# Kernel tuning notes

Hardware: AMD Instinct MI355X
Metric: run time of the kernel (lower is better)

Reference implementation:

```python
import jax, jax.numpy as jnp
import numpy as np
import math

D, H, NQP, NKP = 512, 8, 4, 4
DH = D // H
OUT_DIM = D + H * NKP * 3  # 608


def setup_inputs() -> dict:
    key = jax.random.key(0)
    ks = jax.random.split(key, 12)
    B, L = 2, 1024
    s = jax.random.normal(ks[0], (B, L, D), dtype=jnp.float32)
    R = jax.random.normal(ks[1], (B, L, 3, 3), dtype=jnp.float32)
    tr = jax.random.normal(ks[2], (B, L, 3), dtype=jnp.float32)
    sc = 0.02
    Wq = jax.random.normal(ks[3], (D, D), dtype=jnp.float32) * sc
    Wk = jax.random.normal(ks[4], (D, D), dtype=jnp.float32) * sc
    Wv = jax.random.normal(ks[5], (D, D), dtype=jnp.float32) * sc
    Wqp = jax.random.normal(ks[6], (D, H * NQP * 3), dtype=jnp.float32) * sc
    Wkp = jax.random.normal(ks[7], (D, H * NKP * 3), dtype=jnp.float32) * sc
    Wvp = jax.random.normal(ks[8], (D, H * NKP * 3), dtype=jnp.float32) * sc
    Wo = jax.random.normal(ks[9], (OUT_DIM, D), dtype=jnp.float32) * sc
    bo = jnp.zeros((D,), dtype=jnp.float32)
    gamma = jnp.ones((D,), dtype=jnp.float32)
    beta = jnp.zeros((D,), dtype=jnp.float32)
    w_C = jnp.full((H,), math.log(20.0), dtype=jnp.float32)
    return dict(s=s, R=R, tr=tr, Wq=Wq, Wk=Wk, Wv=Wv, Wqp=Wqp, Wkp=Wkp,
                Wvp=Wvp, Wo=Wo, bo=bo, gamma=gamma, beta=beta, w_C=w_C)


def _layernorm(x, gamma, beta, eps=1e-5):
    mu = jnp.mean(x, axis=-1, keepdims=True)
    var = jnp.var(x, axis=-1, keepdims=True)
    return (x - mu) * jax.lax.rsqrt(var + eps) * gamma + beta


def reference(s, R, tr, Wq, Wk, Wv, Wqp, Wkp, Wvp, Wo, bo, gamma, beta, w_C):
    B, L, _ = s.shape
    # scalar q/k/v: (B, L, H, dh)
    Q = (s @ Wq).reshape(B, L, H, DH)
    K = (s @ Wk).reshape(B, L, H, DH)
    V = (s @ Wv).reshape(B, L, H, DH)
    a_s = jnp.einsum('bihd,bjhd->bhij', Q, K) / math.sqrt(DH)
    # local points: (B, L, H, P, 3)
    Qp = (s @ Wqp).reshape(B, L, H, NQP, 3)
    Kp = (s @ Wkp).reshape(B, L, H, NKP, 3)
    Vp = (s @ Wvp).reshape(B, L, H, NKP, 3)
    tr_e = tr[:, :, None, None, :]
    to_global = lambda p: jnp.einsum('blxy,blhpy->blhpx', R, p) + tr_e
    Qp_g, Kp_g, Vp_g = to_global(Qp), to_global(Kp), to_global(Vp)
    # (B, H, L, P, 3)
    qh = jnp.transpose(Qp_g, (0, 2, 1, 3, 4))
    kh = jnp.transpose(Kp_g, (0, 2, 1, 3, 4))
    diff = qh[:, :, :, None] - kh[:, :, None]          # (B,H,L,L,P,3)
    sq_dist = jnp.sum(diff * diff, axis=(-2, -1))      # (B,H,L,L)
    wc = jax.nn.softplus(w_C)[None, :, None, None]
    attn = jax.nn.softmax(a_s - 0.5 * wc * sq_dist, axis=-1)
    out_s = jnp.einsum('bhij,bjhd->bihd', attn, V).reshape(B, L, D)
    Vp_agg = jnp.einsum('bhij,bjhpc->bihpc', attn, Vp_g)  # (B,L,H,P,3)
    # global -> local: R^T (p - tr)
    Vp_local = jnp.einsum('blyx,blhpy->blhpx', R, Vp_agg - tr_e)
    out_p = Vp_local.reshape(B, L, H * NKP * 3)
    out = jnp.concatenate([out_s, out_p], axis=-1) @ Wo + bo
    return _layernorm(s + out, gamma, beta)
```

## Files before the change

### kernel.cpp

```cpp
#include <hip/hip_runtime.h>
#include <hip/hip_fp16.h>
#include <math.h>

typedef _Float16 f16;
typedef _Float16 f16x8 __attribute__((ext_vector_type(8)));
typedef _Float16 f16x4v __attribute__((ext_vector_type(4)));
typedef float f32x4 __attribute__((ext_vector_type(4)));

#define BATCH   2
#define LSEQ    1024
#define BLTOT   2048
#define DMODEL  512
#define NHEAD   8
#define PDIM    1824
#define AW      96
#define VW      80
#define ODIM    608
#define NSPLIT  2
#define OCPSTR  1310720

__global__ __launch_bounds__(256)
void prep_kernel(const float* __restrict__ Wq, const float* __restrict__ Wk,
                 const float* __restrict__ Wv, const float* __restrict__ Wqp,
                 const float* __restrict__ Wkp, const float* __restrict__ Wvp,
                 const float* __restrict__ Wo,
                 f16* __restrict__ WallT, f16* __restrict__ WoT)
{
    const int blk = blockIdx.x;
    const int t = threadIdx.x;
    __shared__ float tile[32][33];

    if (blk < 912) {
        const int n0 = (blk % 57) * 32, k0 = (blk / 57) * 32;
        const float* src; int ld, nc0;
        if      (n0 < 512)  { src = Wq;  ld = 512; nc0 = n0; }
        else if (n0 < 1024) { src = Wk;  ld = 512; nc0 = n0 - 512; }
        else if (n0 < 1536) { src = Wv;  ld = 512; nc0 = n0 - 1024; }
        else if (n0 < 1632) { src = Wqp; ld = 96;  nc0 = n0 - 1536; }
        else if (n0 < 1728) { src = Wkp; ld = 96;  nc0 = n0 - 1632; }
        else                { src = Wvp; ld = 96;  nc0 = n0 - 1728; }
#pragma unroll
        for (int i = 0; i < 4; ++i) {
            const int idx2 = t + i * 256;
            const int kl = idx2 >> 5, nl = idx2 & 31;
            tile[kl][nl] = src[(long long)(k0 + kl) * ld + nc0 + nl];
        }
        __syncthreads();
#pragma unroll
        for (int i = 0; i < 4; ++i) {
            const int idx2 = t + i * 256;
            const int nl = idx2 >> 5, kl = idx2 & 31;
            WallT[(long long)(n0 + nl) * 512 + k0 + kl] = (f16)tile[kl][nl];
        }
        return;
    }
    {
        const int idx = blk - 912;
        const int n0 = (idx % 16) * 32, k0 = (idx / 16) * 32;
#pragma unroll
        for (int i = 0; i < 4; ++i) {
            const int idx2 = t + i * 256;
            const int kl = idx2 >> 5, nl = idx2 & 31;
            tile[kl][nl] = Wo[(long long)(k0 + kl) * 512 + n0 + nl];
        }
        __syncthreads();
#pragma unroll
        for (int i = 0; i < 4; ++i) {
            const int idx2 = t + i * 256;
            const int nl = idx2 >> 5, kl = idx2 & 31;
            WoT[(long long)(n0 + nl) * 608 + k0 + kl] = (f16)tile[kl][nl];
        }
    }
}

__global__ __launch_bounds__(256)
void proj_kernel(const float* __restrict__ s, const f16* __restrict__ WallT,
                 f16* __restrict__ P)
{
    __shared__ f16 As[2][128][40];
    __shared__ f16 Bs[2][96][40];
    const int t = threadIdx.x;
    const int w = t >> 6, lane = t & 63, l15 = lane & 15, lhi = lane >> 4;
    const int row0 = blockIdx.y * 128, col0 = blockIdx.x * 96;

    f32x4 acc[2][6];
#pragma unroll
    for (int m = 0; m < 2; ++m)
#pragma unroll
        for (int n = 0; n < 6; ++n) acc[m][n] = (f32x4){0.f, 0.f, 0.f, 0.f};

    float4 aR[2][2];
    f16x8 bR[2];

#pragma unroll
    for (int i = 0; i < 2; ++i) {
        const int cid = t + i * 256;
        const int r = cid >> 2, c = cid & 3;
        aR[i][0] = *(const float4*)&s[(long long)(row0 + r) * 512 + c * 8];
        aR[i][1] = *(const float4*)&s[(long long)(row0 + r) * 512 + c * 8 + 4];
    }
#pragma unroll
    for (int i = 0; i < 2; ++i) {
        const int cid = t + i * 256;
        if (cid < 384) {
            const int br = cid >> 2, bc = cid & 3;
            bR[i] = *(const f16x8*)&WallT[(long long)(col0 + br) * 512 + bc * 8];
        }
    }
#pragma unroll
    for (int i = 0; i < 2; ++i) {
        const int cid = t + i * 256;
        const int r = cid >> 2, c = cid & 3;
        f16x8 v = { (f16)aR[i][0].x, (f16)aR[i][0].y, (f16)aR[i][0].z, (f16)aR[i][0].w,
                    (f16)aR[i][1].x, (f16)aR[i][1].y, (f16)aR[i][1].z, (f16)aR[i][1].w };
        *(f16x8*)&As[0][r][c * 8] = v;
    }
#pragma unroll
    for (int i = 0; i < 2; ++i) {
        const int cid = t + i * 256;
        if (cid < 384) *(f16x8*)&Bs[0][cid >> 2][(cid & 3) * 8] = bR[i];
    }
    __syncthreads();

    for (int st = 0; st < 16; ++st) {
        const int cur = st & 1;
        if (st + 1 < 16) {
            const int k0 = (st + 1) << 5;
#pragma unroll
            for (int i = 0; i < 2; ++i) {
                const int cid = t + i * 256;
                const int r = cid >> 2, c = cid & 3;
                aR[i][0] = *(const float4*)&s[(long long)(row0 + r) * 512 + k0 + c * 8];
                aR[i][1] = *(const float4*)&s[(long long)(row0 + r) * 512 + k0 + c * 8 + 4];
            }
#pragma unroll
            for (int i = 0; i < 2; ++i) {
                const int cid = t + i * 256;
                if (cid < 384) {
                    const int br = cid >> 2, bc = cid & 3;
                    bR[i] = *(const f16x8*)&WallT[(long long)(col0 + br) * 512 + k0 + bc * 8];
                }
            }
        }
        f16x8 af[2], bf[6];
#pragma unroll
        for (int m = 0; m < 2; ++m)
            af[m] = *(const f16x8*)&As[cur][w * 32 + m * 16 + l15][lhi * 8];
#pragma unroll
        for (int n = 0; n < 6; ++n)
            bf[n] = *(const f16x8*)&Bs[cur][n * 16 + l15][lhi * 8];
#pragma unroll
        for (int m = 0; m < 2; ++m)
#pragma unroll
            for (int n = 0; n < 6; ++n)
                acc[m][n] = __builtin_amdgcn_mfma_f32_16x16x32_f16(af[m], bf[n], acc[m][n], 0, 0, 0);
        if (st + 1 < 16) {
#pragma unroll
            for (int i = 0; i < 2; ++i) {
                const int cid = t + i * 256;
                const int r = cid >> 2, c = cid & 3;
                f16x8 v = { (f16)aR[i][0].x, (f16)aR[i][0].y, (f16)aR[i][0].z, (f16)aR[i][0].w,
                            (f16)aR[i][1].x, (f16)aR[i][1].y, (f16)aR[i][1].z, (f16)aR[i][1].w };
                *(f16x8*)&As[cur ^ 1][r][c * 8] = v;
            }
#pragma unroll
            for (int i = 0; i < 2; ++i) {
                const int cid = t + i * 256;
                if (cid < 384) *(f16x8*)&Bs[cur ^ 1][cid >> 2][(cid & 3) * 8] = bR[i];
            }
        }
        __syncthreads();
    }

#pragma unroll
    for (int m = 0; m < 2; ++m) {
        const int row = row0 + w * 32 + m * 16 + lhi * 4;
#pragma unroll
        for (int n = 0; n < 6; ++n) {
            const int col = col0 + n * 16 + l15;
#pragma unroll
            for (int r = 0; r < 4; ++r)
                P[(long long)(row + r) * PDIM + col] = (f16)acc[m][n][r];
        }
    }
}

__global__ __launch_bounds__(256)
void build_aug2_kernel(const f16* __restrict__ P, const float* __restrict__ Rm,
                       const float* __restrict__ tr, const float* __restrict__ wC,
                       f16* __restrict__ QA, f16* __restrict__ KA,
                       f16* __restrict__ VCT, float* __restrict__ KOFF)
{
    const int l0 = blockIdx.x * 64;
    const int bh = blockIdx.y;
    const int b = bh >> 3, h = bh & 7;
    const int t = threadIdx.x;

    __shared__ float Rl[64][9];
    __shared__ float trl[64][3];
    __shared__ f16 gq[64][12];
    __shared__ f16 gk[64][12];
    __shared__ float k2[64][4];
    __shared__ f16 Vt[VW][72];
    __shared__ float wcs;

    const long long blbase = (long long)b * LSEQ + l0;

    for (int i = t; i < 64 * 9; i += 256) Rl[i / 9][i % 9] = Rm[blbase * 9 + i];
    for (int i = t; i < 64 * 3; i += 256) trl[i / 3][i % 3] = tr[blbase * 3 + i];
    if (t == 0) { float x = wC[h]; wcs = log1pf(expf(x)); }
    __syncthreads();
    const float wc = wcs;

    for (int i = t; i < 768; i += 256) {
        const int l = i / 12, pp = i - l * 12;
        const int proj = pp >> 2, p = pp & 3;
        const f16* src = P + (blbase + l) * PDIM + 1536 + proj * 96 + h * 12 + p * 3;
        const float x = (float)src[0], y = (float)src[1], z = (float)src[2];
        const float gx = Rl[l][0]*x + Rl[l][1]*y + Rl[l][2]*z + trl[l][0];
        const float gy = Rl[l][3]*x + Rl[l][4]*y + Rl[l][5]*z + trl[l][1];
        const float gz = Rl[l][6]*x + Rl[l][7]*y + Rl[l][8]*z + trl[l][2];
        if (proj == 0) {
            gq[l][p * 3 + 0] = (f16)(wc * gx);
            gq[l][p * 3 + 1] = (f16)(wc * gy);
            gq[l][p * 3 + 2] = (f16)(wc * gz);
        } else if (proj == 1) {
            gk[l][p * 3 + 0] = (f16)gx;
            gk[l][p * 3 + 1] = (f16)gy;
            gk[l][p * 3 + 2] = (f16)gz;
            k2[l][p] = gx * gx + gy * gy + gz * gz;
        } else {
            Vt[64 + p * 3 + 0][l] = (f16)gx;
            Vt[64 + p * 3 + 1][l] = (f16)gy;
            Vt[64 + p * 3 + 2][l] = (f16)gz;
        }
    }
    for (int i = t; i < 512; i += 256) {
        const int l = i >> 3, ch = i & 7;
        f16x8 v = *(const f16x8*)&P[(blbase + l) * PDIM + 1024 + h * 64 + ch * 8];
#pragma unroll
        for (int j = 0; j < 8; ++j) Vt[ch * 8 + j][l] = v[j];
    }
    for (int i = t; i < 36; i += 256) {
        const int r = 76 + i / 9, ch = i % 9;
        *(f16x8*)&Vt[r][ch * 8] = (f16x8){0,0,0,0,0,0,0,0};
    }
    __syncthreads();

    if (t < 64)
        KOFF[(long long)bh * LSEQ + l0 + t] =
            0.5f * wc * (k2[t][0] + k2[t][1] + k2[t][2] + k2[t][3]);

    for (int i = t; i < 768; i += 256) {
        const int l = i / 12, ch = i - l * 12;
        const long long prow = (blbase + l) * PDIM;
        const long long orow = ((long long)bh * LSEQ + l0 + l) * AW;
        f16x8 q, k;
        if (ch < 8) {
            f16x8 qv = *(const f16x8*)&P[prow + h * 64 + ch * 8];
            f16x8 kv = *(const f16x8*)&P[prow + 512 + h * 64 + ch * 8];
            q = qv * (f16)0.125f;
            k = kv;
        } else if (ch == 8) {
#pragma unroll
            for (int j = 0; j < 8; ++j) { q[j] = gq[l][j]; k[j] = gk[l][j]; }
        } else if (ch == 9) {
#pragma unroll
            for (int j = 0; j < 8; ++j) {
                q[j] = (j < 4) ? gq[l][8 + j] : (f16)0.f;
                k[j] = (j < 4) ? gk[l][8 + j] : (f16)0.f;
            }
        } else {
            q = (f16x8){0,0,0,0,0,0,0,0};
            k = (f16x8){0,0,0,0,0,0,0,0};
        }
        *(f16x8*)&QA[orow + ch * 8] = q;
        *(f16x8*)&KA[orow + ch * 8] = k;
    }
    for (int i = t; i < 640; i += 256) {
        const int c = i >> 3, lg = i & 7;
        *(f16x8*)&VCT[((long long)bh * VW + c) * LSEQ + l0 + lg * 8] =
            *(const f16x8*)&Vt[c][lg * 8];
    }
}

__global__ __launch_bounds__(256, 2)
void attn_kernel(const f16* __restrict__ QA, const f16* __restrict__ KA,
                 const f16* __restrict__ VCT, const float* __restrict__ KOFF,
                 f16* __restrict__ OCp, float* __restrict__ LSE)
{
    const int bh = blockIdx.y;
    const int q0 = blockIdx.x * 64;
    const int z  = blockIdx.z;
    const int t = threadIdx.x;
    const int w = t >> 6, lane = t & 63, l15 = lane & 15, lhi = lane >> 4;

    __shared__ f16 Ks[128][104];
    __shared__ f16 Vs[VW][136];
    __shared__ f16 Ps[64][136];

    const f16* qbase = QA + ((long long)bh * LSEQ + q0 + w * 16 + l15) * AW;
    f16x8 qf[3];
#pragma unroll
    for (int ks = 0; ks < 3; ++ks)
        qf[ks] = *(const f16x8*)(qbase + ks * 32 + lhi * 8);

    f32x4 Oacc[5];
#pragma unroll
    for (int nv = 0; nv < 5; ++nv) Oacc[nv] = (f32x4){0.f, 0.f, 0.f, 0.f};
    float M[4], L[4];
#pragma unroll
    for (int r = 0; r < 4; ++r) { M[r] = -1e30f; L[r] = 0.f; }

    const f16* kgbase = KA + (long long)bh * LSEQ * AW;
    const f16* vgbase = VCT + (long long)bh * VW * LSEQ;
    const float* koffb = KOFF + (long long)bh * LSEQ;

    const int kvbeg = z * (LSEQ / NSPLIT);
    const int kvend = kvbeg + LSEQ / NSPLIT;

#pragma unroll
    for (int i = 0; i < 6; ++i) {
        const int cid = t + i * 256;
        const int r = cid / 12, c = cid - r * 12;
        *(f16x8*)&Ks[r][c * 8] = *(const f16x8*)(kgbase + (long long)(kvbeg + r) * AW + c * 8);
    }
#pragma unroll
    for (int i = 0; i < 5; ++i) {
        const int cid = t + i * 256;
        const int r = cid >> 4, c = cid & 15;
        *(f16x8*)&Vs[r][c * 8] = *(const f16x8*)(vgbase + (long long)r * LSEQ + kvbeg + c * 8);
    }
    __syncthreads();

    for (int kv0 = kvbeg; kv0 < kvend; kv0 += 128) {
        const bool more = (kv0 + 128 < kvend);
        f16x8 kpre[6], vpre[5];
        if (more) {
#pragma unroll
            for (int i = 0; i < 6; ++i) {
                const int cid = t + i * 256;
                const int r = cid / 12, c = cid - r * 12;
                kpre[i] = *(const f16x8*)(kgbase + (long long)(kv0 + 128 + r) * AW + c * 8);
            }
#pragma unroll
            for (int i = 0; i < 5; ++i) {
                const int cid = t + i * 256;
                const int r = cid >> 4, c = cid & 15;
                vpre[i] = *(const f16x8*)(vgbase + (long long)r * LSEQ + kv0 + 128 + c * 8);
            }
        }

        f32x4 sc[8];
#pragma unroll
        for (int n = 0; n < 8; ++n) sc[n] = (f32x4){0.f, 0.f, 0.f, 0.f};
        __builtin_amdgcn_s_setprio(1);
#pragma unroll
        for (int n = 0; n < 8; ++n)
#pragma unroll
            for (int ks = 0; ks < 3; ++ks) {
                f16x8 kb = *(const f16x8*)&Ks[n * 16 + l15][ks * 32 + lhi * 8];
                sc[n] = __builtin_amdgcn_mfma_f32_16x16x32_f16(qf[ks], kb, sc[n], 0, 0, 0);
            }
        __builtin_amdgcn_s_setprio(0);
#pragma unroll
        for (int n = 0; n < 8; ++n) {
            const float ko = koffb[kv0 + n * 16 + l15];
#pragma unroll
            for (int r = 0; r < 4; ++r) sc[n][r] -= ko;
        }
        float mr[4];
#pragma unroll
        for (int r = 0; r < 4; ++r) {
            float m = sc[0][r];
#pragma unroll
            for (int n = 1; n < 8; ++n) m = fmaxf(m, sc[n][r]);
#pragma unroll
            for (int off = 1; off < 16; off <<= 1) m = fmaxf(m, __shfl_xor(m, off));
            mr[r] = m;
        }
        const bool nog = (mr[0] <= M[0] + 8.f) && (mr[1] <= M[1] + 8.f) &&
                         (mr[2] <= M[2] + 8.f) && (mr[3] <= M[3] + 8.f);
        float rsum[4] = {0.f, 0.f, 0.f, 0.f};
        if (__all(nog)) {
#pragma unroll
            for (int n = 0; n < 8; ++n)
#pragma unroll
                for (int r = 0; r < 4; ++r) {
                    const float p = __expf(sc[n][r] - M[r]);
                    sc[n][r] = p;
                    rsum[r] += p;
                }
#pragma unroll
            for (int r = 0; r < 4; ++r) {
                float s2 = rsum[r];
#pragma unroll
                for (int off = 1; off < 16; off <<= 1) s2 += __shfl_xor(s2, off);
                L[r] += s2;
            }
        } else {
            float sscale[4];
#pragma unroll
            for (int r = 0; r < 4; ++r) {
                const float nm = fmaxf(M[r], mr[r]);
                sscale[r] = __expf(M[r] - nm);
                M[r] = nm;
            }
#pragma unroll
            for (int n = 0; n < 8; ++n)
#pragma unroll
                for (int r = 0; r < 4; ++r) {
                    const float p = __expf(sc[n][r] - M[r]);
                    sc[n][r] = p;
                    rsum[r] += p;
                }
#pragma unroll
            for (int r = 0; r < 4; ++r) {
                float s2 = rsum[r];
#pragma unroll
                for (int off = 1; off < 16; off <<= 1) s2 += __shfl_xor(s2, off);
                L[r] = L[r] * sscale[r] + s2;
            }
#pragma unroll
            for (int nv = 0; nv < 5; ++nv)
#pragma unroll
                for (int r = 0; r < 4; ++r) Oacc[nv][r] *= sscale[r];
        }

#pragma unroll
        for (int n = 0; n < 8; ++n)
#pragma unroll
            for (int r = 0; r < 4; ++r)
                Ps[w * 16 + lhi * 4 + r][n * 16 + l15] = (f16)sc[n][r];

        f16x8 pa[4];
#pragma unroll
        for (int ks = 0; ks < 4; ++ks)
            pa[ks] = *(const f16x8*)&Ps[w * 16 + l15][ks * 32 + lhi * 8];
        __builtin_amdgcn_s_setprio(1);
#pragma unroll
        for (int nv = 0; nv < 5; ++nv)
#pragma unroll
            for (int ks = 0; ks < 4; ++ks) {
                f16x8 vb = *(const f16x8*)&Vs[nv * 16 + l15][ks * 32 + lhi * 8];
                Oacc[nv] = __builtin_amdgcn_mfma_f32_16x16x32_f16(pa[ks], vb, Oacc[nv], 0, 0, 0);
            }
        __builtin_amdgcn_s_setprio(0);
        __syncthreads();

        if (more) {
#pragma unroll
            for (int i = 0; i < 6; ++i) {
                const int cid = t + i * 256;
                const int r = cid / 12, c = cid - r * 12;
                *(f16x8*)&Ks[r][c * 8] = kpre[i];
            }
#pragma unroll
            for (int i = 0; i < 5; ++i) {
                const int cid = t + i * 256;
                const int r = cid >> 4, c = cid & 15;
                *(f16x8*)&Vs[r][c * 8] = vpre[i];
            }
        }
        __syncthreads();
    }

    float inv[4];
#pragma unroll
    for (int r = 0; r < 4; ++r) inv[r] = 1.0f / L[r];
    f16* obase = OCp + (((long long)(z * 16 + bh) * LSEQ) + q0 + w * 16 + lhi * 4) * VW;
#pragma unroll
    for (int nv = 0; nv < 5; ++nv)
#pragma unroll
        for (int r = 0; r < 4; ++r)
            obase[r * VW + nv * 16 + l15] = (f16)(Oacc[nv][r] * inv[r]);
    if (l15 == 0) {
#pragma unroll
        for (int r = 0; r < 4; ++r)
            LSE[(long long)(z * 16 + bh) * LSEQ + q0 + w * 16 + lhi * 4 + r] =
                M[r] + __logf(L[r]);
    }
}

__global__ __launch_bounds__(256)
void combine_concat_kernel(const f16* __restrict__ OCp, const float* __restrict__ LSE,
                           const float* __restrict__ Rm, const float* __restrict__ tr,
                           f16* __restrict__ CC)
{
    const int bl0 = blockIdx.x * 4;
    const int b = bl0 >> 10;
    const int t = threadIdx.x;

    __shared__ float w1s[4][8], w2s[4][8];
    if (t < 32) {
        const int row = t >> 3, h = t & 7;
        const int l = (bl0 + row) & 1023;
        const int bh = b * 8 + h;
        const float l1 = LSE[(long long)bh * LSEQ + l];
        const float l2 = LSE[(long long)(16 + bh) * LSEQ + l];
        const float mm = fmaxf(l1, l2);
        const float e1 = __expf(l1 - mm), e2 = __expf(l2 - mm);
        const float inv = 1.0f / (e1 + e2);
        w1s[row][h] = e1 * inv; w2s[row][h] = e2 * inv;
    }
    __syncthreads();

    for (int idx = t; idx < 2048; idx += 256) {
        const int row = idx >> 9, c = idx & 511;
        const int h = c >> 6, ch = c & 63;
        const int l = (bl0 + row) & 1023;
        const long long base = ((long long)(b * 8 + h) * LSEQ + l) * VW + ch;
        const float v = w1s[row][h] * (float)OCp[base] + w2s[row][h] * (float)OCp[OCPSTR + base];
        CC[(long long)(bl0 + row) * ODIM + c] = (f16)v;
    }
    if (t < 128) {
        const int row = t >> 5, h = (t >> 2) & 7, p = t & 3;
        const int bl = bl0 + row, l = bl & 1023;
        const long long base = ((long long)(b * 8 + h) * LSEQ + l) * VW + 64 + p * 3;
        const float w1 = w1s[row][h], w2 = w2s[row][h];
        float o[3];
#pragma unroll
        for (int c = 0; c < 3; ++c)
            o[c] = w1 * (float)OCp[base + c] + w2 * (float)OCp[OCPSTR + base + c]
                 - tr[(long long)bl * 3 + c];
        const float* Rr = Rm + (long long)bl * 9;
        f16* crow = CC + (long long)bl * ODIM + 512 + h * 12 + p * 3;
        crow[0] = (f16)(Rr[0]*o[0] + Rr[3]*o[1] + Rr[6]*o[2]);
        crow[1] = (f16)(Rr[1]*o[0] + Rr[4]*o[1] + Rr[7]*o[2]);
        crow[2] = (f16)(Rr[2]*o[0] + Rr[5]*o[1] + Rr[8]*o[2]);
    }
}

__global__ __launch_bounds__(256)
void out_gemm_kernel(const f16* __restrict__ CC, const f16* __restrict__ WoT,
                     float* __restrict__ Y)
{
    __shared__ f16 As[2][64][40];
    __shared__ f16 Bs[2][64][40];
    const int t = threadIdx.x;
    const int w = t >> 6, lane = t & 63, l15 = lane & 15, lhi = lane >> 4;
    const int wr = w >> 1, wc = w & 1;
    const int row0 = blockIdx.y * 64, col0 = blockIdx.x * 64;
    const int ar = t >> 2, ac = t & 3;

    f32x4 acc[2][2];
#pragma unroll
    for (int m = 0; m < 2; ++m)
#pragma unroll
        for (int n = 0; n < 2; ++n) acc[m][n] = (f32x4){0.f, 0.f, 0.f, 0.f};

    f16x8 aR, bR;
    aR = *(const f16x8*)&CC[(long long)(row0 + ar) * ODIM + ac * 8];
    bR = *(const f16x8*)&WoT[(long long)(col0 + ar) * ODIM + ac * 8];
    *(f16x8*)&As[0][ar][ac * 8] = aR;
    *(f16x8*)&Bs[0][ar][ac * 8] = bR;
    __syncthreads();

    for (int st = 0; st < 19; ++st) {
        const int cur = st & 1;
        if (st + 1 < 19) {
            const int k0 = (st + 1) << 5;
            aR = *(const f16x8*)&CC[(long long)(row0 + ar) * ODIM + k0 + ac * 8];
            bR = *(const f16x8*)&WoT[(long long)(col0 + ar) * ODIM + k0 + ac * 8];
        }
        f16x8 af[2], bf[2];
#pragma unroll
        for (int m = 0; m < 2; ++m)
            af[m] = *(const f16x8*)&As[cur][wr * 32 + m * 16 + l15][lhi * 8];
#pragma unroll
        for (int n = 0; n < 2; ++n)
            bf[n] = *(const f16x8*)&Bs[cur][wc * 32 + n * 16 + l15][lhi * 8];
#pragma unroll
        for (int m = 0; m < 2; ++m)
#pragma unroll
            for (int n = 0; n < 2; ++n)
                acc[m][n] = __builtin_amdgcn_mfma_f32_16x16x32_f16(af[m], bf[n], acc[m][n], 0, 0, 0);
        if (st + 1 < 19) {
            *(f16x8*)&As[cur ^ 1][ar][ac * 8] = aR;
            *(f16x8*)&Bs[cur ^ 1][ar][ac * 8] = bR;
        }
        __syncthreads();
    }

#pragma unroll
    for (int m = 0; m < 2; ++m) {
        const int row = row0 + wr * 32 + m * 16 + lhi * 4;
#pragma unroll
        for (int n = 0; n < 2; ++n) {
            const int col = col0 + wc * 32 + n * 16 + l15;
#pragma unroll
            for (int r = 0; r < 4; ++r)
                Y[(long long)(row + r) * 512 + col] = acc[m][n][r];
        }
    }
}

__global__ __launch_bounds__(256)
void residual_ln_kernel(const float* __restrict__ s, const float* __restrict__ Y,
                        const float* __restrict__ bo, const float* __restrict__ gamma,
                        const float* __restrict__ beta, float* __restrict__ out)
{
    const int bl = blockIdx.x;
    const int t = threadIdx.x;
    const float* srow = s + (long long)bl * DMODEL;
    const float* yrow = Y + (long long)bl * DMODEL;

    const float v0 = srow[t]       + yrow[t]       + bo[t];
    const float v1 = srow[t + 256] + yrow[t + 256] + bo[t + 256];

    float sum = v0 + v1, sq = v0 * v0 + v1 * v1;
#pragma unroll
    for (int o = 32; o > 0; o >>= 1) {
        sum += __shfl_xor(sum, o);
        sq  += __shfl_xor(sq,  o);
    }
    __shared__ float rs[4], rq[4];
    const int wid = t >> 6, lane = t & 63;
    if (lane == 0) { rs[wid] = sum; rq[wid] = sq; }
    __syncthreads();
    sum = rs[0] + rs[1] + rs[2] + rs[3];
    sq  = rq[0] + rq[1] + rq[2] + rq[3];

    const float mu  = sum * (1.0f / DMODEL);
    const float var = sq * (1.0f / DMODEL) - mu * mu;
    const float inv = rsqrtf(var + 1e-5f);

    out[(long long)bl * DMODEL + t]       = (v0 - mu) * inv * gamma[t]       + beta[t];
    out[(long long)bl * DMODEL + t + 256] = (v1 - mu) * inv * gamma[t + 256] + beta[t + 256];
}

extern "C" void kernel_launch(void* const* d_in, const int* in_sizes, int n_in,
                              void* d_out, int out_size, void* d_ws, size_t ws_size,
                              hipStream_t stream)
{
    const float* s    = (const float*)d_in[0];
    const float* R    = (const float*)d_in[1];
    const float* tr   = (const float*)d_in[2];
    const float* Wq   = (const float*)d_in[3];
    const float* Wk   = (const float*)d_in[4];
    const float* Wv   = (const float*)d_in[5];
    const float* Wqp  = (const float*)d_in[6];
    const float* Wkp  = (const float*)d_in[7];
    const float* Wvp  = (const float*)d_in[8];
    const float* Wo   = (const float*)d_in[9];
    const float* bo   = (const float*)d_in[10];
    const float* gam  = (const float*)d_in[11];
    const float* bet  = (const float*)d_in[12];
    const float* wC   = (const float*)d_in[13];
    float* out = (float*)d_out;

    f16* WallT = (f16*)d_ws;
    f16* WoT   = WallT + 933888;
    f16* P     = WoT + 311296;
    f16* QA    = P + 3735552;
    f16* KA    = QA + 1572864;
    f16* VCT   = KA + 1572864;
    float* KOFF = (float*)(VCT + 1310720);
    f16* OCp    = (f16*)(KOFF + 16384);
    float* LSE  = (float*)(OCp + 2621440);
    f16* CC     = (f16*)(LSE + 32768);
    float* Y    = (float*)(CC + 1245184);

    const dim3 blk(256);

    prep_kernel<<<dim3(1216), blk, 0, stream>>>(Wq, Wk, Wv, Wqp, Wkp, Wvp, Wo,
                                                WallT, WoT);

    proj_kernel<<<dim3(19, 16), blk, 0, stream>>>(s, WallT, P);

    build_aug2_kernel<<<dim3(16, 16), blk, 0, stream>>>(P, R, tr, wC, QA, KA, VCT, KOFF);

    attn_kernel<<<dim3(16, 16, NSPLIT), blk, 0, stream>>>(QA, KA, VCT, KOFF, OCp, LSE);

    combine_concat_kernel<<<dim3(512), blk, 0, stream>>>(OCp, LSE, R, tr, CC);

    out_gemm_kernel<<<dim3(8, 32), blk, 0, stream>>>(CC, WoT, Y);

    residual_ln_kernel<<<dim3(BLTOT), blk, 0, stream>>>(s, Y, bo, gam, bet, out);
}
```

Measured before the change: 74.19 us.

## Fuse weight prep into GEMMs and merge split-KV attention with combine

Removes the separate weight transpose/convert kernel: the projection and output GEMMs now load fp32 weights directly and transpose-convert into shared memory per tile. The attention kernel runs both KV halves in one 512-thread block, two groups of four waves. The halves are merged in shared memory and the concat output, including the rotation back to local frames, is written directly. This drops the combine kernel and the partial-output round trip. Costs are scattered 2-byte shared stores for the weight transpose and a larger shared-memory footprint per attention block, which may lower occupancy.

```diff
diff --git a/kernel.cpp b/kernel.cpp
--- a/kernel.cpp
+++ b/kernel.cpp
@@ -16,65 +16,12 @@
 #define AW      96
 #define VW      80
 #define ODIM    608
-#define NSPLIT  2
-#define OCPSTR  1310720
 
 __global__ __launch_bounds__(256)
-void prep_kernel(const float* __restrict__ Wq, const float* __restrict__ Wk,
+void proj_kernel(const float* __restrict__ s,
+                 const float* __restrict__ Wq, const float* __restrict__ Wk,
                  const float* __restrict__ Wv, const float* __restrict__ Wqp,
                  const float* __restrict__ Wkp, const float* __restrict__ Wvp,
-                 const float* __restrict__ Wo,
-                 f16* __restrict__ WallT, f16* __restrict__ WoT)
-{
-    const int blk = blockIdx.x;
-    const int t = threadIdx.x;
-    __shared__ float tile[32][33];
-
-    if (blk < 912) {
-        const int n0 = (blk % 57) * 32, k0 = (blk / 57) * 32;
-        const float* src; int ld, nc0;
-        if      (n0 < 512)  { src = Wq;  ld = 512; nc0 = n0; }
-        else if (n0 < 1024) { src = Wk;  ld = 512; nc0 = n0 - 512; }
-        else if (n0 < 1536) { src = Wv;  ld = 512; nc0 = n0 - 1024; }
-        else if (n0 < 1632) { src = Wqp; ld = 96;  nc0 = n0 - 1536; }
-        else if (n0 < 1728) { src = Wkp; ld = 96;  nc0 = n0 - 1632; }
-        else                { src = Wvp; ld = 96;  nc0 = n0 - 1728; }
-#pragma unroll
-        for (int i = 0; i < 4; ++i) {
-            const int idx2 = t + i * 256;
-            const int kl = idx2 >> 5, nl = idx2 & 31;
-            tile[kl][nl] = src[(long long)(k0 + kl) * ld + nc0 + nl];
-        }
-        __syncthreads();
-#pragma unroll
-        for (int i = 0; i < 4; ++i) {
-            const int idx2 = t + i * 256;
-            const int nl = idx2 >> 5, kl = idx2 & 31;
-            WallT[(long long)(n0 + nl) * 512 + k0 + kl] = (f16)tile[kl][nl];
-        }
-        return;
-    }
-    {
-        const int idx = blk - 912;
-        const int n0 = (idx % 16) * 32, k0 = (idx / 16) * 32;
-#pragma unroll
-        for (int i = 0; i < 4; ++i) {
-            const int idx2 = t + i * 256;
-            const int kl = idx2 >> 5, nl = idx2 & 31;
-            tile[kl][nl] = Wo[(long long)(k0 + kl) * 512 + n0 + nl];
-        }
-        __syncthreads();
-#pragma unroll
-        for (int i = 0; i < 4; ++i) {
-            const int idx2 = t + i * 256;
-            const int nl = idx2 >> 5, kl = idx2 & 31;
-            WoT[(long long)(n0 + nl) * 608 + k0 + kl] = (f16)tile[kl][nl];
-        }
-    }
-}
-
-__global__ __launch_bounds__(256)
-void proj_kernel(const float* __restrict__ s, const f16* __restrict__ WallT,
                  f16* __restrict__ P)
 {
     __shared__ f16 As[2][128][40];
@@ -83,14 +30,29 @@
     const int w = t >> 6, lane = t & 63, l15 = lane & 15, lhi = lane >> 4;
     const int row0 = blockIdx.y * 128, col0 = blockIdx.x * 96;
 
+    const float* bsrc[3]; int bld[3], bkk[3], bnn[3];
+#pragma unroll
+    for (int i = 0; i < 3; ++i) {
+        const int cid = t + i * 256;
+        const int kk = cid / 24, c4 = cid % 24;
+        const int n = col0 + c4 * 4;
+        const float* src; int nc, ld;
+        if      (n < 512)  { src = Wq;  nc = n;        ld = 512; }
+        else if (n < 1024) { src = Wk;  nc = n - 512;  ld = 512; }
+        else if (n < 1536) { src = Wv;  nc = n - 1024; ld = 512; }
+        else if (n < 1632) { src = Wqp; nc = n - 1536; ld = 96; }
+        else if (n < 1728) { src = Wkp; nc = n - 1632; ld = 96; }
+        else               { src = Wvp; nc = n - 1728; ld = 96; }
+        bsrc[i] = src + nc; bld[i] = ld; bkk[i] = kk; bnn[i] = c4 * 4;
+    }
+
     f32x4 acc[2][6];
 #pragma unroll
     for (int m = 0; m < 2; ++m)
 #pragma unroll
         for (int n = 0; n < 6; ++n) acc[m][n] = (f32x4){0.f, 0.f, 0.f, 0.f};
 
-    float4 aR[2][2];
-    f16x8 bR[2];
+    float4 aR[2][2], bpre[3];
 
 #pragma unroll
     for (int i = 0; i < 2; ++i) {
@@ -100,13 +62,8 @@
         aR[i][1] = *(const float4*)&s[(long long)(row0 + r) * 512 + c * 8 + 4];
     }
 #pragma unroll
-    for (int i = 0; i < 2; ++i) {
-        const int cid = t + i * 256;
-        if (cid < 384) {
-            const int br = cid >> 2, bc = cid & 3;
-            bR[i] = *(const f16x8*)&WallT[(long long)(col0 + br) * 512 + bc * 8];
-        }
-    }
+    for (int i = 0; i < 3; ++i)
+        bpre[i] = *(const float4*)&bsrc[i][(long long)bkk[i] * bld[i]];
 #pragma unroll
     for (int i = 0; i < 2; ++i) {
         const int cid = t + i * 256;
@@ -116,9 +73,11 @@
         *(f16x8*)&As[0][r][c * 8] = v;
     }
 #pragma unroll
-    for (int i = 0; i < 2; ++i) {
-        const int cid = t + i * 256;
-        if (cid < 384) *(f16x8*)&Bs[0][cid >> 2][(cid & 3) * 8] = bR[i];
+    for (int i = 0; i < 3; ++i) {
+        Bs[0][bnn[i] + 0][bkk[i]] = (f16)bpre[i].x;
+        Bs[0][bnn[i] + 1][bkk[i]] = (f16)bpre[i].y;
+        Bs[0][bnn[i] + 2][bkk[i]] = (f16)bpre[i].z;
+        Bs[0][bnn[i] + 3][bkk[i]] = (f16)bpre[i].w;
     }
     __syncthreads();
 
@@ -134,13 +93,8 @@
                 aR[i][1] = *(const float4*)&s[(long long)(row0 + r) * 512 + k0 + c * 8 + 4];
             }
 #pragma unroll
-            for (int i = 0; i < 2; ++i) {
-                const int cid = t + i * 256;
-                if (cid < 384) {
-                    const int br = cid >> 2, bc = cid & 3;
-                    bR[i] = *(const f16x8*)&WallT[(long long)(col0 + br) * 512 + k0 + bc * 8];
-                }
-            }
+            for (int i = 0; i < 3; ++i)
+                bpre[i] = *(const float4*)&bsrc[i][(long long)(k0 + bkk[i]) * bld[i]];
         }
         f16x8 af[2], bf[6];
 #pragma unroll
@@ -164,9 +118,11 @@
                 *(f16x8*)&As[cur ^ 1][r][c * 8] = v;
             }
 #pragma unroll
-            for (int i = 0; i < 2; ++i) {
-                const int cid = t + i * 256;
-                if (cid < 384) *(f16x8*)&Bs[cur ^ 1][cid >> 2][(cid & 3) * 8] = bR[i];
+            for (int i = 0; i < 3; ++i) {
+                Bs[cur ^ 1][bnn[i] + 0][bkk[i]] = (f16)bpre[i].x;
+                Bs[cur ^ 1][bnn[i] + 1][bkk[i]] = (f16)bpre[i].y;
+                Bs[cur ^ 1][bnn[i] + 2][bkk[i]] = (f16)bpre[i].z;
+                Bs[cur ^ 1][bnn[i] + 3][bkk[i]] = (f16)bpre[i].w;
             }
         }
         __syncthreads();
@@ -284,22 +240,34 @@
     }
 }
 
-__global__ __launch_bounds__(256, 2)
-void attn_kernel(const f16* __restrict__ QA, const f16* __restrict__ KA,
-                 const f16* __restrict__ VCT, const float* __restrict__ KOFF,
-                 f16* __restrict__ OCp, float* __restrict__ LSE)
+__global__ __launch_bounds__(512, 2)
+void attn8_kernel(const f16* __restrict__ QA, const f16* __restrict__ KA,
+                  const f16* __restrict__ VCT, const float* __restrict__ KOFF,
+                  const float* __restrict__ Rm, const float* __restrict__ trv,
+                  f16* __restrict__ CC)
 {
     const int bh = blockIdx.y;
     const int q0 = blockIdx.x * 64;
-    const int z  = blockIdx.z;
+    const int b = bh >> 3, h = bh & 7;
     const int t = threadIdx.x;
-    const int w = t >> 6, lane = t & 63, l15 = lane & 15, lhi = lane >> 4;
-
-    __shared__ f16 Ks[128][104];
-    __shared__ f16 Vs[VW][136];
-    __shared__ f16 Ps[64][136];
-
-    const f16* qbase = QA + ((long long)bh * LSEQ + q0 + w * 16 + l15) * AW;
+    const int w = t >> 6;
+    const int g = w >> 2;
+    const int wsub = w & 3;
+    const int lane = t & 63, l15 = lane & 15, lhi = lane >> 4;
+    const int tg = t & 255;
+
+    __shared__ f16 Ks[2][128][104];
+    __shared__ f16 Vs[2][VW][136];
+    __shared__ f16 Ps[2][64][136];
+    __shared__ float Rtr[64][12];
+
+    const long long blbase = (long long)b * LSEQ + q0;
+    for (int i = t; i < 64 * 12; i += 512) {
+        const int row = i / 12, c = i % 12;
+        Rtr[row][c] = (c < 9) ? Rm[(blbase + row) * 9 + c] : trv[(blbase + row) * 3 + (c - 9)];
+    }
+
+    const f16* qbase = QA + ((long long)bh * LSEQ + q0 + wsub * 16 + l15) * AW;
     f16x8 qf[3];
 #pragma unroll
     for (int ks = 0; ks < 3; ++ks)
@@ -316,36 +284,36 @@
     const f16* vgbase = VCT + (long long)bh * VW * LSEQ;
     const float* koffb = KOFF + (long long)bh * LSEQ;
 
-    const int kvbeg = z * (LSEQ / NSPLIT);
-    const int kvend = kvbeg + LSEQ / NSPLIT;
+    const int kvbeg = g * 512;
 
 #pragma unroll
     for (int i = 0; i < 6; ++i) {
-        const int cid = t + i * 256;
+        const int cid = tg + i * 256;
         const int r = cid / 12, c = cid - r * 12;
-        *(f16x8*)&Ks[r][c * 8] = *(const f16x8*)(kgbase + (long long)(kvbeg + r) * AW + c * 8);
+        *(f16x8*)&Ks[g][r][c * 8] = *(const f16x8*)(kgbase + (long long)(kvbeg + r) * AW + c * 8);
     }
 #pragma unroll
     for (int i = 0; i < 5; ++i) {
-        const int cid = t + i * 256;
+        const int cid = tg + i * 256;
         const int r = cid >> 4, c = cid & 15;
-        *(f16x8*)&Vs[r][c * 8] = *(const f16x8*)(vgbase + (long long)r * LSEQ + kvbeg + c * 8);
-    }
-    __syncthreads();
-
-    for (int kv0 = kvbeg; kv0 < kvend; kv0 += 128) {
-        const bool more = (kv0 + 128 < kvend);
+        *(f16x8*)&Vs[g][r][c * 8] = *(const f16x8*)(vgbase + (long long)r * LSEQ + kvbeg + c * 8);
+    }
+    __syncthreads();
+
+    for (int it = 0; it < 4; ++it) {
+        const int kv0 = kvbeg + it * 128;
+        const bool more = (it < 3);
         f16x8 kpre[6], vpre[5];
         if (more) {
 #pragma unroll
             for (int i = 0; i < 6; ++i) {
-                const int cid = t + i * 256;
+                const int cid = tg + i * 256;
                 const int r = cid / 12, c = cid - r * 12;
                 kpre[i] = *(const f16x8*)(kgbase + (long long)(kv0 + 128 + r) * AW + c * 8);
             }
 #pragma unroll
             for (int i = 0; i < 5; ++i) {
-                const int cid = t + i * 256;
+                const int cid = tg + i * 256;
                 const int r = cid >> 4, c = cid & 15;
                 vpre[i] = *(const f16x8*)(vgbase + (long long)r * LSEQ + kv0 + 128 + c * 8);
             }
@@ -359,7 +327,7 @@
         for (int n = 0; n < 8; ++n)
 #pragma unroll
             for (int ks = 0; ks < 3; ++ks) {
-                f16x8 kb = *(const f16x8*)&Ks[n * 16 + l15][ks * 32 + lhi * 8];
+                f16x8 kb = *(const f16x8*)&Ks[g][n * 16 + l15][ks * 32 + lhi * 8];
                 sc[n] = __builtin_amdgcn_mfma_f32_16x16x32_f16(qf[ks], kb, sc[n], 0, 0, 0);
             }
         __builtin_amdgcn_s_setprio(0);
@@ -431,18 +399,18 @@
         for (int n = 0; n < 8; ++n)
 #pragma unroll
             for (int r = 0; r < 4; ++r)
-                Ps[w * 16 + lhi * 4 + r][n * 16 + l15] = (f16)sc[n][r];
+                Ps[g][wsub * 16 + lhi * 4 + r][n * 16 + l15] = (f16)sc[n][r];
 
         f16x8 pa[4];
 #pragma unroll
         for (int ks = 0; ks < 4; ++ks)
-            pa[ks] = *(const f16x8*)&Ps[w * 16 + l15][ks * 32 + lhi * 8];
+            pa[ks] = *(const f16x8*)&Ps[g][wsub * 16 + l15][ks * 32 + lhi * 8];
         __builtin_amdgcn_s_setprio(1);
 #pragma unroll
         for (int nv = 0; nv < 5; ++nv)
 #pragma unroll
             for (int ks = 0; ks < 4; ++ks) {
-                f16x8 vb = *(const f16x8*)&Vs[nv * 16 + l15][ks * 32 + lhi * 8];
+                f16x8 vb = *(const f16x8*)&Vs[g][nv * 16 + l15][ks * 32 + lhi * 8];
                 Oacc[nv] = __builtin_amdgcn_mfma_f32_16x16x32_f16(pa[ks], vb, Oacc[nv], 0, 0, 0);
             }
         __builtin_amdgcn_s_setprio(0);
@@ -451,88 +419,69 @@
         if (more) {
 #pragma unroll
             for (int i = 0; i < 6; ++i) {
-                const int cid = t + i * 256;
+                const int cid = tg + i * 256;
                 const int r = cid / 12, c = cid - r * 12;
-                *(f16x8*)&Ks[r][c * 8] = kpre[i];
+                *(f16x8*)&Ks[g][r][c * 8] = kpre[i];
             }
 #pragma unroll
             for (int i = 0; i < 5; ++i) {
-                const int cid = t + i * 256;
+                const int cid = tg + i * 256;
                 const int r = cid >> 4, c = cid & 15;
-                *(f16x8*)&Vs[r][c * 8] = vpre[i];
+                *(f16x8*)&Vs[g][r][c * 8] = vpre[i];
             }
         }
         __syncthreads();
     }
 
-    float inv[4];
-#pragma unroll
-    for (int r = 0; r < 4; ++r) inv[r] = 1.0f / L[r];
-    f16* obase = OCp + (((long long)(z * 16 + bh) * LSEQ) + q0 + w * 16 + lhi * 4) * VW;
-#pragma unroll
-    for (int nv = 0; nv < 5; ++nv)
-#pragma unroll
-        for (int r = 0; r < 4; ++r)
-            obase[r * VW + nv * 16 + l15] = (f16)(Oacc[nv][r] * inv[r]);
-    if (l15 == 0) {
-#pragma unroll
-        for (int r = 0; r < 4; ++r)
-            LSE[(long long)(z * 16 + bh) * LSEQ + q0 + w * 16 + lhi * 4 + r] =
-                M[r] + __logf(L[r]);
+    float* O1  = (float*)&Ks[0][0][0];
+    float* ML1 = O1 + 64 * VW;
+    if (g == 1) {
+#pragma unroll
+        for (int r = 0; r < 4; ++r) {
+            const int i = wsub * 16 + lhi * 4 + r;
+#pragma unroll
+            for (int nv = 0; nv < 5; ++nv)
+                O1[i * VW + nv * 16 + l15] = Oacc[nv][r];
+            if (l15 == 0) { ML1[i * 2 + 0] = M[r]; ML1[i * 2 + 1] = L[r]; }
+        }
+    }
+    __syncthreads();
+
+    float* opbuf = (float*)&Vs[0][0][0];
+    if (g == 0) {
+#pragma unroll
+        for (int r = 0; r < 4; ++r) {
+            const int i = wsub * 16 + lhi * 4 + r;
+            const float m1 = ML1[i * 2 + 0], l1 = ML1[i * 2 + 1];
+            const float nm = fmaxf(M[r], m1);
+            const float a0 = __expf(M[r] - nm), a1 = __expf(m1 - nm);
+            const float inv = 1.0f / (L[r] * a0 + l1 * a1);
+            f16* crow = CC + (blbase + i) * ODIM;
+#pragma unroll
+            for (int nv = 0; nv < 4; ++nv) {
+                const float val = (Oacc[nv][r] * a0 + O1[i * VW + nv * 16 + l15] * a1) * inv;
+                crow[h * 64 + nv * 16 + l15] = (f16)val;
+            }
+            const float val4 = (Oacc[4][r] * a0 + O1[i * VW + 64 + l15] * a1) * inv;
+            if (l15 < 12) opbuf[i * 12 + l15] = val4;
+        }
+    }
+    __syncthreads();
+
+    if (t < 256) {
+        const int i = t >> 2, p = t & 3;
+        const float ox = opbuf[i * 12 + p * 3 + 0] - Rtr[i][9];
+        const float oy = opbuf[i * 12 + p * 3 + 1] - Rtr[i][10];
+        const float oz = opbuf[i * 12 + p * 3 + 2] - Rtr[i][11];
+        f16* crow = CC + (blbase + i) * ODIM + 512 + h * 12 + p * 3;
+        crow[0] = (f16)(Rtr[i][0]*ox + Rtr[i][3]*oy + Rtr[i][6]*oz);
+        crow[1] = (f16)(Rtr[i][1]*ox + Rtr[i][4]*oy + Rtr[i][7]*oz);
+        crow[2] = (f16)(Rtr[i][2]*ox + Rtr[i][5]*oy + Rtr[i][8]*oz);
     }
 }
 
 __global__ __launch_bounds__(256)
-void combine_concat_kernel(const f16* __restrict__ OCp, const float* __restrict__ LSE,
-                           const float* __restrict__ Rm, const float* __restrict__ tr,
-                           f16* __restrict__ CC)
-{
-    const int bl0 = blockIdx.x * 4;
-    const int b = bl0 >> 10;
-    const int t = threadIdx.x;
-
-    __shared__ float w1s[4][8], w2s[4][8];
-    if (t < 32) {
-        const int row = t >> 3, h = t & 7;
-        const int l = (bl0 + row) & 1023;
-        const int bh = b * 8 + h;
-        const float l1 = LSE[(long long)bh * LSEQ + l];
-        const float l2 = LSE[(long long)(16 + bh) * LSEQ + l];
-        const float mm = fmaxf(l1, l2);
-        const float e1 = __expf(l1 - mm), e2 = __expf(l2 - mm);
-        const float inv = 1.0f / (e1 + e2);
-        w1s[row][h] = e1 * inv; w2s[row][h] = e2 * inv;
-    }
-    __syncthreads();
-
-    for (int idx = t; idx < 2048; idx += 256) {
-        const int row = idx >> 9, c = idx & 511;
-        const int h = c >> 6, ch = c & 63;
-        const int l = (bl0 + row) & 1023;
-        const long long base = ((long long)(b * 8 + h) * LSEQ + l) * VW + ch;
-        const float v = w1s[row][h] * (float)OCp[base] + w2s[row][h] * (float)OCp[OCPSTR + base];
-        CC[(long long)(bl0 + row) * ODIM + c] = (f16)v;
-    }
-    if (t < 128) {
-        const int row = t >> 5, h = (t >> 2) & 7, p = t & 3;
-        const int bl = bl0 + row, l = bl & 1023;
-        const long long base = ((long long)(b * 8 + h) * LSEQ + l) * VW + 64 + p * 3;
-        const float w1 = w1s[row][h], w2 = w2s[row][h];
-        float o[3];
-#pragma unroll
-        for (int c = 0; c < 3; ++c)
-            o[c] = w1 * (float)OCp[base + c] + w2 * (float)OCp[OCPSTR + base + c]
-                 - tr[(long long)bl * 3 + c];
-        const float* Rr = Rm + (long long)bl * 9;
-        f16* crow = CC + (long long)bl * ODIM + 512 + h * 12 + p * 3;
-        crow[0] = (f16)(Rr[0]*o[0] + Rr[3]*o[1] + Rr[6]*o[2]);
-        crow[1] = (f16)(Rr[1]*o[0] + Rr[4]*o[1] + Rr[7]*o[2]);
-        crow[2] = (f16)(Rr[2]*o[0] + Rr[5]*o[1] + Rr[8]*o[2]);
-    }
-}
-
-__global__ __launch_bounds__(256)
-void out_gemm_kernel(const f16* __restrict__ CC, const f16* __restrict__ WoT,
+void out_gemm_kernel(const f16* __restrict__ CC, const float* __restrict__ Wo,
                      float* __restrict__ Y)
 {
     __shared__ f16 As[2][64][40];
@@ -543,17 +492,31 @@
     const int row0 = blockIdx.y * 64, col0 = blockIdx.x * 64;
     const int ar = t >> 2, ac = t & 3;
 
+    const int bkk0 = t >> 4, bnn0 = (t & 15) * 4;
+    const int bkk1 = (t + 256) >> 4, bnn1 = (t & 15) * 4;
+
     f32x4 acc[2][2];
 #pragma unroll
     for (int m = 0; m < 2; ++m)
 #pragma unroll
         for (int n = 0; n < 2; ++n) acc[m][n] = (f32x4){0.f, 0.f, 0.f, 0.f};
 
-    f16x8 aR, bR;
+    f16x8 aR;
+    float4 bpre[2];
     aR = *(const f16x8*)&CC[(long long)(row0 + ar) * ODIM + ac * 8];
-    bR = *(const f16x8*)&WoT[(long long)(col0 + ar) * ODIM + ac * 8];
+    bpre[0] = *(const float4*)&Wo[(long long)bkk0 * 512 + col0 + bnn0];
+    bpre[1] = *(const float4*)&Wo[(long long)bkk1 * 512 + col0 + bnn1];
     *(f16x8*)&As[0][ar][ac * 8] = aR;
-    *(f16x8*)&Bs[0][ar][ac * 8] = bR;
+    {
+        Bs[0][bnn0 + 0][bkk0] = (f16)bpre[0].x;
+        Bs[0][bnn0 + 1][bkk0] = (f16)bpre[0].y;
+        Bs[0][bnn0 + 2][bkk0] = (f16)bpre[0].z;
+        Bs[0][bnn0 + 3][bkk0] = (f16)bpre[0].w;
+        Bs[0][bnn1 + 0][bkk1] = (f16)bpre[1].x;
+        Bs[0][bnn1 + 1][bkk1] = (f16)bpre[1].y;
+        Bs[0][bnn1 + 2][bkk1] = (f16)bpre[1].z;
+        Bs[0][bnn1 + 3][bkk1] = (f16)bpre[1].w;
+    }
     __syncthreads();
 
     for (int st = 0; st < 19; ++st) {
@@ -561,7 +524,8 @@
         if (st + 1 < 19) {
             const int k0 = (st + 1) << 5;
             aR = *(const f16x8*)&CC[(long long)(row0 + ar) * ODIM + k0 + ac * 8];
-            bR = *(const f16x8*)&WoT[(long long)(col0 + ar) * ODIM + k0 + ac * 8];
+            bpre[0] = *(const float4*)&Wo[(long long)(k0 + bkk0) * 512 + col0 + bnn0];
+            bpre[1] = *(const float4*)&Wo[(long long)(k0 + bkk1) * 512 + col0 + bnn1];
         }
         f16x8 af[2], bf[2];
 #pragma unroll
@@ -577,7 +541,14 @@
                 acc[m][n] = __builtin_amdgcn_mfma_f32_16x16x32_f16(af[m], bf[n], acc[m][n], 0, 0, 0);
         if (st + 1 < 19) {
             *(f16x8*)&As[cur ^ 1][ar][ac * 8] = aR;
-            *(f16x8*)&Bs[cur ^ 1][ar][ac * 8] = bR;
+            Bs[cur ^ 1][bnn0 + 0][bkk0] = (f16)bpre[0].x;
+            Bs[cur ^ 1][bnn0 + 1][bkk0] = (f16)bpre[0].y;
+            Bs[cur ^ 1][bnn0 + 2][bkk0] = (f16)bpre[0].z;
+            Bs[cur ^ 1][bnn0 + 3][bkk0] = (f16)bpre[0].w;
+            Bs[cur ^ 1][bnn1 + 0][bkk1] = (f16)bpre[1].x;
+            Bs[cur ^ 1][bnn1 + 1][bkk1] = (f16)bpre[1].y;
+            Bs[cur ^ 1][bnn1 + 2][bkk1] = (f16)bpre[1].z;
+            Bs[cur ^ 1][bnn1 + 3][bkk1] = (f16)bpre[1].w;
         }
         __syncthreads();
     }
@@ -649,32 +620,23 @@
     const float* wC   = (const float*)d_in[13];
     float* out = (float*)d_out;
 
-    f16* WallT = (f16*)d_ws;
-    f16* WoT   = WallT + 933888;
-    f16* P     = WoT + 311296;
+    f16* P     = (f16*)d_ws;
     f16* QA    = P + 3735552;
     f16* KA    = QA + 1572864;
     f16* VCT   = KA + 1572864;
     float* KOFF = (float*)(VCT + 1310720);
-    f16* OCp    = (f16*)(KOFF + 16384);
-    float* LSE  = (float*)(OCp + 2621440);
-    f16* CC     = (f16*)(LSE + 32768);
+    f16* CC     = (f16*)(KOFF + 16384);
     float* Y    = (float*)(CC + 1245184);
 
     const dim3 blk(256);
 
-    prep_kernel<<<dim3(1216), blk, 0, stream>>>(Wq, Wk, Wv, Wqp, Wkp, Wvp, Wo,
-                                                WallT, WoT);
-
-    proj_kernel<<<dim3(19, 16), blk, 0, stream>>>(s, WallT, P);
+    proj_kernel<<<dim3(19, 16), blk, 0, stream>>>(s, Wq, Wk, Wv, Wqp, Wkp, Wvp, P);
 
     build_aug2_kernel<<<dim3(16, 16), blk, 0, stream>>>(P, R, tr, wC, QA, KA, VCT, KOFF);
 
-    attn_kernel<<<dim3(16, 16, NSPLIT), blk, 0, stream>>>(QA, KA, VCT, KOFF, OCp, LSE);
-
-    combine_concat_kernel<<<dim3(512), blk, 0, stream>>>(OCp, LSE, R, tr, CC);
-
-    out_gemm_kernel<<<dim3(8, 32), blk, 0, stream>>>(CC, WoT, Y);
+    attn8_kernel<<<dim3(16, 16), dim3(512), 0, stream>>>(QA, KA, VCT, KOFF, R, tr, CC);
+
+    out_gemm_kernel<<<dim3(8, 32), blk, 0, stream>>>(CC, Wo, Y);
 
     residual_ln_kernel<<<dim3(BLTOT), blk, 0, stream>>>(s, Y, bo, gam, bet, out);
 }
```

New measurement: 82.11 us. 1.11x slower.
